# Performance work log

Hardware: AMD Instinct MI355X
Metric: run time of the kernel (lower is better)

The kernel has to match this reference:

```python
import jax, jax.numpy as jnp
import numpy as np

B = 1024      # batch
E = 1024      # encoding_dim
OUT = 34      # 17 joints x 2 coords


def setup_inputs() -> dict:
    key = jax.random.key(0)
    ks = jax.random.split(key, 8)
    s = 0.02  # weight init scale
    return {
        "h": jax.random.normal(ks[0], (B, E), dtype=jnp.float32),
        "c": jax.random.normal(ks[1], (B, E), dtype=jnp.float32),
        "W_ih": jax.random.normal(ks[2], (4 * E, E), dtype=jnp.float32) * s,
        "W_hh": jax.random.normal(ks[3], (4 * E, E), dtype=jnp.float32) * s,
        "b_ih": jax.random.normal(ks[4], (4 * E,), dtype=jnp.float32) * s,
        "b_hh": jax.random.normal(ks[5], (4 * E,), dtype=jnp.float32) * s,
        "W_out": jax.random.normal(ks[6], (OUT, E), dtype=jnp.float32) * s,
        "b_out": jax.random.normal(ks[7], (OUT,), dtype=jnp.float32) * s,
        "future_preds": 10,
    }


def reference(h, c, W_ih, W_hh, b_ih, b_hh, W_out, b_out, future_preds):
    E_ = h.shape[1]
    start = jnp.zeros_like(h)  # zeros=True start token

    def step(carry, _):
        h_t, c_t, x = carry
        # LSTMCell: gates in PyTorch order i, f, g, o
        gates = x @ W_ih.T + b_ih + h_t @ W_hh.T + b_hh  # [B, 4E]
        i = jax.nn.sigmoid(gates[:, 0 * E_:1 * E_])
        f = jax.nn.sigmoid(gates[:, 1 * E_:2 * E_])
        g = jnp.tanh(gates[:, 2 * E_:3 * E_])
        o = jax.nn.sigmoid(gates[:, 3 * E_:4 * E_])
        c_new = f * c_t + i * g
        h_new = o * jnp.tanh(c_new)
        return (h_new, c_new, h_new), h_new

    _, hs = jax.lax.scan(step, (h, c, start), None, length=future_preds)
    # hs: [T, B, E] -> [B, T, E]
    preds = jnp.transpose(hs, (1, 0, 2))
    return preds @ W_out.T + b_out  # [B, T, 34]
```

## Files before the change

### kernel.cpp

```cpp
#include <hip/hip_runtime.h>
#include <cstdint>
#include <cstddef>

#define E_DIM   1024
#define B_DIM   1024
#define T_STEPS 10
#define OUT_DIM 34
#define OUT_PAD 48
#define HSTR    24
#define QK      256
#define WQ_ELEMS (64 * QK)
#define DYN_LDS (2 * WQ_ELEMS * 2 + 128 * HSTR * 2)

typedef __attribute__((ext_vector_type(4))) float  f32x4;
typedef __attribute__((ext_vector_type(8))) __bf16 bf16x8;

__device__ __forceinline__ unsigned short f2bf(float f) {
    unsigned int u = __float_as_uint(f);
    u = (u + 0x7FFFu + ((u >> 16) & 1u)) >> 16;
    return (unsigned short)u;
}
__device__ __forceinline__ float sigmoid_(float x) { return 1.0f / (1.0f + __expf(-x)); }
__device__ __forceinline__ float tanh_(float x)    { return 2.0f / (1.0f + __expf(-2.0f * x)) - 1.0f; }

__global__ void prep_weights_frag(const float* __restrict__ W_ih, const float* __restrict__ W_hh,
                                  unsigned short* __restrict__ WsumF, unsigned short* __restrict__ WhhF) {
    const int bn = blockIdx.x >> 2, qtr = blockIdx.x & 3;
    const int nt = threadIdx.x >> 6, lane = threadIdx.x & 63;
    const int j = lane & 15, q = lane >> 4;
    const int srow = nt * E_DIM + bn * 16 + j;
    const float* wi = W_ih + (size_t)srow * E_DIM;
    const float* wh = W_hh + (size_t)srow * E_DIM;
    const size_t dstb = (size_t)bn * 65536 + (size_t)qtr * 16384 + nt * 512 + lane * 8;
#pragma unroll
    for (int ks8 = 0; ks8 < 8; ++ks8) {
        const int k = qtr * 256 + ks8 * 32 + q * 8;
        float4 i0 = *(const float4*)(wi + k);
        float4 i1 = *(const float4*)(wi + k + 4);
        float4 h0 = *(const float4*)(wh + k);
        float4 h1 = *(const float4*)(wh + k + 4);
        unsigned short* ds = WsumF + dstb + ks8 * 2048;
        unsigned short* dh = WhhF  + dstb + ks8 * 2048;
        ds[0] = f2bf(i0.x + h0.x); ds[1] = f2bf(i0.y + h0.y);
        ds[2] = f2bf(i0.z + h0.z); ds[3] = f2bf(i0.w + h0.w);
        ds[4] = f2bf(i1.x + h1.x); ds[5] = f2bf(i1.y + h1.y);
        ds[6] = f2bf(i1.z + h1.z); ds[7] = f2bf(i1.w + h1.w);
        dh[0] = f2bf(h0.x); dh[1] = f2bf(h0.y); dh[2] = f2bf(h0.z); dh[3] = f2bf(h0.w);
        dh[4] = f2bf(h1.x); dh[5] = f2bf(h1.y); dh[6] = f2bf(h1.z); dh[7] = f2bf(h1.w);
    }
}

__global__ void prep_state(const float* __restrict__ h0, const float* __restrict__ W_out,
                           const float* __restrict__ b_ih, const float* __restrict__ b_hh,
                           unsigned short* __restrict__ hbuf, unsigned short* __restrict__ Woutp,
                           float* __restrict__ bperm) {
    const int b = blockIdx.x;
    const int t = threadIdx.x;
    if (b < 1024) {
        const size_t i = ((size_t)b * 256 + t) * 4;
        float4 hv = *(const float4*)(h0 + i);
        hbuf[i + 0] = f2bf(hv.x);
        hbuf[i + 1] = f2bf(hv.y);
        hbuf[i + 2] = f2bf(hv.z);
        hbuf[i + 3] = f2bf(hv.w);
    } else if (b < 1072) {
        const int o = b - 1024;
        const int k = t * 4;
        float4 w = make_float4(0.f, 0.f, 0.f, 0.f);
        if (o < OUT_DIM) w = *(const float4*)(W_out + (size_t)o * E_DIM + k);
        const size_t dst = (size_t)o * E_DIM + k;
        Woutp[dst + 0] = f2bf(w.x);
        Woutp[dst + 1] = f2bf(w.y);
        Woutp[dst + 2] = f2bf(w.z);
        Woutp[dst + 3] = f2bf(w.w);
    } else {
        const int n = (b - 1072) * 256 + t;
        const int g = (n >> 4) & 3;
        const int e = ((n >> 6) << 4) | (n & 15);
        const int srow = g * E_DIM + e;
        bperm[n] = b_ih[srow] + b_hh[srow];
    }
}

__global__ void prep_c(const float* __restrict__ c0, float* __restrict__ C) {
    const int m = blockIdx.x;
    const int e0 = threadIdx.x * 4;
    float4 v = *(const float4*)(c0 + (size_t)m * E_DIM + e0);
    const int bm = m >> 7, wave = (m >> 5) & 3, mt = (m >> 4) & 1, q = (m >> 2) & 3, r = m & 3;
    const float vv[4] = {v.x, v.y, v.z, v.w};
#pragma unroll
    for (int ii = 0; ii < 4; ++ii) {
        const int e = e0 + ii;
        const int bn = e >> 4, j = e & 15;
        const int lane = q * 16 + j;
        C[(((size_t)(bn * 8 + bm) * 4 + wave) * 64 + lane) * 8 + mt * 4 + r] = vv[ii];
    }
}

__global__ __launch_bounds__(256, 2) void lstm_step(
    const unsigned short* __restrict__ WF,
    const float* __restrict__ bp,
    const unsigned short* __restrict__ Hin,
    float* __restrict__ C,
    unsigned short* __restrict__ Hout)
{
    extern __shared__ __align__(16) unsigned short smem[];
    unsigned short* Wbuf0 = smem;
    unsigned short* Wbuf1 = smem + WQ_ELEMS;
    unsigned short* Ht    = smem + 2 * WQ_ELEMS;

    const int tid  = threadIdx.x;
    const int wave = tid >> 6;
    const int lane = tid & 63;
    const int bn = blockIdx.x;
    const int bm = blockIdx.y;
    const int j  = lane & 15;
    const int q  = lane >> 4;

    f32x4 acc[2][4];
#pragma unroll
    for (int a = 0; a < 2; ++a)
#pragma unroll
        for (int b = 0; b < 4; ++b) acc[a][b] = (f32x4){0.f, 0.f, 0.f, 0.f};

    const int nb = bn * 64 + j;
    const float bi = bp[nb +  0];
    const float bf = bp[nb + 16];
    const float bg = bp[nb + 32];
    const float bo = bp[nb + 48];
    const size_t cbase = (((size_t)(bn * 8 + bm) * 4 + wave) * 64 + lane) * 8;
    float4 cold0 = *(const float4*)(C + cbase);
    float4 cold1 = *(const float4*)(C + cbase + 4);

    const unsigned short* arow0 = Hin + (size_t)(bm * 128 + wave * 32 + j) * E_DIM + q * 8;
    const unsigned short* arow1 = arow0 + (size_t)16 * E_DIM;
    const unsigned short* wsrc  = WF + (size_t)bn * 65536;

    uint4 ra[8][2];
#pragma unroll
    for (int p = 0; p < 8; ++p) {
        ra[p][0] = *(const uint4*)(arow0 + p * 32);
        ra[p][1] = *(const uint4*)(arow1 + p * 32);
    }

    uint4 wreg[8];
#pragma unroll
    for (int i = 0; i < 8; ++i)
        wreg[i] = *(const uint4*)(wsrc + (i * 256 + tid) * 8);
#pragma unroll
    for (int i = 0; i < 8; ++i)
        *(uint4*)(Wbuf0 + (i * 256 + tid) * 8) = wreg[i];
    __syncthreads();

    for (int qtr = 0; qtr < 4; ++qtr) {
        if (qtr < 3) {
#pragma unroll
            for (int i = 0; i < 8; ++i)
                wreg[i] = *(const uint4*)(wsrc + (size_t)(qtr + 1) * WQ_ELEMS + (i * 256 + tid) * 8);
        }
        const unsigned short* wb = ((qtr & 1) ? Wbuf1 : Wbuf0) + lane * 8;
#pragma unroll
        for (int ks8 = 0; ks8 < 8; ++ks8) {
            const int ks = qtr * 8 + ks8;
            bf16x8 av0 = __builtin_bit_cast(bf16x8, ra[ks8][0]);
            bf16x8 av1 = __builtin_bit_cast(bf16x8, ra[ks8][1]);
            bf16x8 bv[4];
#pragma unroll
            for (int nt = 0; nt < 4; ++nt)
                bv[nt] = *(const bf16x8*)(wb + (ks8 * 4 + nt) * 512);
#pragma unroll
            for (int nt = 0; nt < 4; ++nt) {
                acc[0][nt] = __builtin_amdgcn_mfma_f32_16x16x32_bf16(av0, bv[nt], acc[0][nt], 0, 0, 0);
                acc[1][nt] = __builtin_amdgcn_mfma_f32_16x16x32_bf16(av1, bv[nt], acc[1][nt], 0, 0, 0);
            }
            if (ks < 24) {
                ra[ks8][0] = *(const uint4*)(arow0 + (ks + 8) * 32);
                ra[ks8][1] = *(const uint4*)(arow1 + (ks + 8) * 32);
            }
        }
        if (qtr < 3) {
            unsigned short* wn_ = ((qtr + 1) & 1) ? Wbuf1 : Wbuf0;
#pragma unroll
            for (int i = 0; i < 8; ++i)
                *(uint4*)(wn_ + (i * 256 + tid) * 8) = wreg[i];
            __syncthreads();
        }
    }

    float4 cnew[2];
    const float coldv[2][4] = {{cold0.x, cold0.y, cold0.z, cold0.w},
                               {cold1.x, cold1.y, cold1.z, cold1.w}};
#pragma unroll
    for (int mt = 0; mt < 2; ++mt) {
#pragma unroll
        for (int r = 0; r < 4; ++r) {
            const float iv = sigmoid_(acc[mt][0][r] + bi);
            const float fv = sigmoid_(acc[mt][1][r] + bf);
            const float gv = tanh_(acc[mt][2][r] + bg);
            const float ov = sigmoid_(acc[mt][3][r] + bo);
            const float cn = fv * coldv[mt][r] + iv * gv;
            cnew[mt][r] = cn;
            const int rowl = wave * 32 + mt * 16 + q * 4 + r;
            Ht[rowl * HSTR + j] = f2bf(ov * tanh_(cn));
        }
    }
    *(float4*)(C + cbase)     = cnew[0];
    *(float4*)(C + cbase + 4) = cnew[1];
    __syncthreads();

    {
        const int row = tid >> 1, part = tid & 1;
        uint4 v = *(const uint4*)(Ht + row * HSTR + part * 8);
        *(uint4*)(Hout + (size_t)(bm * 128 + row) * E_DIM + bn * 16 + part * 8) = v;
    }
}

__global__ __launch_bounds__(256) void proj_kernel(
    const unsigned short* __restrict__ Hs,
    const unsigned short* __restrict__ Wo,
    const float* __restrict__ b_out,
    float* __restrict__ Out)
{
    __shared__ float red[4][32][OUT_PAD];

    const int tid = threadIdx.x, wave = tid >> 6, lane = tid & 63;
    const int j = lane & 15, q = lane >> 4;
    const int t  = blockIdx.y;
    const int bb = blockIdx.x;
    const unsigned short* Hbase = Hs + ((size_t)t * B_DIM + (size_t)bb * 32) * E_DIM;
    const int k0 = wave * 256;

    f32x4 acc[2][3];
#pragma unroll
    for (int a = 0; a < 2; ++a)
#pragma unroll
        for (int b = 0; b < 3; ++b) acc[a][b] = (f32x4){0.f, 0.f, 0.f, 0.f};

#pragma unroll
    for (int kk = 0; kk < 256; kk += 32) {
        const int kc = k0 + kk + q * 8;
        bf16x8 av[2], bv[3];
#pragma unroll
        for (int mt = 0; mt < 2; ++mt)
            av[mt] = *(const bf16x8*)(Hbase + (size_t)(mt * 16 + j) * E_DIM + kc);
#pragma unroll
        for (int nt = 0; nt < 3; ++nt)
            bv[nt] = *(const bf16x8*)(Wo + (size_t)(nt * 16 + j) * E_DIM + kc);
#pragma unroll
        for (int mt = 0; mt < 2; ++mt)
#pragma unroll
            for (int nt = 0; nt < 3; ++nt)
                acc[mt][nt] = __builtin_amdgcn_mfma_f32_16x16x32_bf16(av[mt], bv[nt], acc[mt][nt], 0, 0, 0);
    }

#pragma unroll
    for (int mt = 0; mt < 2; ++mt)
#pragma unroll
        for (int nt = 0; nt < 3; ++nt)
#pragma unroll
            for (int r = 0; r < 4; ++r)
                red[wave][mt * 16 + q * 4 + r][nt * 16 + j] = acc[mt][nt][r];
    __syncthreads();

#pragma unroll
    for (int ii = 0; ii < 6; ++ii) {
        const int idx = tid * 6 + ii;
        const int row = idx / OUT_PAD, o = idx % OUT_PAD;
        if (o < OUT_DIM) {
            const float s = red[0][row][o] + red[1][row][o] + red[2][row][o] + red[3][row][o];
            Out[((size_t)(bb * 32 + row) * T_STEPS + t) * OUT_DIM + o] = s + b_out[o];
        }
    }
}

extern "C" void kernel_launch(void* const* d_in, const int* in_sizes, int n_in,
                              void* d_out, int out_size, void* d_ws, size_t ws_size,
                              hipStream_t stream) {
    (void)in_sizes; (void)n_in; (void)out_size; (void)ws_size;
    const float* h     = (const float*)d_in[0];
    const float* c     = (const float*)d_in[1];
    const float* W_ih  = (const float*)d_in[2];
    const float* W_hh  = (const float*)d_in[3];
    const float* b_ih  = (const float*)d_in[4];
    const float* b_hh  = (const float*)d_in[5];
    const float* W_out = (const float*)d_in[6];
    const float* b_out = (const float*)d_in[7];
    float* out = (float*)d_out;

    char* ws = (char*)d_ws;
    unsigned short* WsumF = (unsigned short*)(ws + 0);
    unsigned short* WhhF  = (unsigned short*)(ws + 8388608);
    float*          bperm = (float*)(ws + 16777216);
    unsigned short* Woutp = (unsigned short*)(ws + 16842752);
    float*          cbuf  = (float*)(ws + 16941056);
    unsigned short* hs    = (unsigned short*)(ws + 21135360);

    hipFuncSetAttribute((const void*)lstm_step,
                        hipFuncAttributeMaxDynamicSharedMemorySize, DYN_LDS);

    prep_weights_frag<<<256, 256, 0, stream>>>(W_ih, W_hh, WsumF, WhhF);
    prep_state<<<1088, 256, 0, stream>>>(h, W_out, b_ih, b_hh, hs, Woutp, bperm);
    prep_c<<<1024, 256, 0, stream>>>(c, cbuf);

    lstm_step<<<dim3(64, 8), 256, DYN_LDS, stream>>>(WhhF, bperm, hs, cbuf,
                                                     hs + (size_t)B_DIM * E_DIM);
    for (int t = 1; t < T_STEPS; ++t)
        lstm_step<<<dim3(64, 8), 256, DYN_LDS, stream>>>(WsumF, bperm,
                                                         hs + (size_t)t * B_DIM * E_DIM,
                                                         cbuf,
                                                         hs + (size_t)(t + 1) * B_DIM * E_DIM);

    proj_kernel<<<dim3(32, T_STEPS), 256, 0, stream>>>(hs + (size_t)B_DIM * E_DIM,
                                                       Woutp, b_out, out);
}
```

Before: 329.5 us.

## Use eight smaller K-stages with double-buffered A registers and vectorized weight prep

Splits the recurrent GEMM's K loop into eight 128-wide stages instead of four 256-wide ones, halving the LDS weight buffers and the weight registers held per stage. Activation fragments are now double-buffered in registers per stage rather than refilled one slot at a time. The weight prep kernel writes packed 16-byte stores and uses twice as many blocks. The smaller LDS footprint lets the explicit max-dynamic-shared-memory attribute be dropped, though it adds more barriers per kernel.

```diff
diff --git a/kernel.cpp b/kernel.cpp
--- a/kernel.cpp
+++ b/kernel.cpp
@@ -8,9 +8,10 @@
 #define OUT_DIM 34
 #define OUT_PAD 48
 #define HSTR    24
-#define QK      256
-#define WQ_ELEMS (64 * QK)
-#define DYN_LDS (2 * WQ_ELEMS * 2 + 128 * HSTR * 2)
+#define EK      128
+#define WE_ELEMS (64 * EK)
+#define DYN_LDS (2 * WE_ELEMS * 2 + 128 * HSTR * 2)
+#define LDP     40
 
 typedef __attribute__((ext_vector_type(4))) float  f32x4;
 typedef __attribute__((ext_vector_type(8))) __bf16 bf16x8;
@@ -25,28 +26,29 @@
 
 __global__ void prep_weights_frag(const float* __restrict__ W_ih, const float* __restrict__ W_hh,
                                   unsigned short* __restrict__ WsumF, unsigned short* __restrict__ WhhF) {
-    const int bn = blockIdx.x >> 2, qtr = blockIdx.x & 3;
+    const int bn = blockIdx.x >> 3, E = blockIdx.x & 7;
     const int nt = threadIdx.x >> 6, lane = threadIdx.x & 63;
     const int j = lane & 15, q = lane >> 4;
     const int srow = nt * E_DIM + bn * 16 + j;
     const float* wi = W_ih + (size_t)srow * E_DIM;
     const float* wh = W_hh + (size_t)srow * E_DIM;
-    const size_t dstb = (size_t)bn * 65536 + (size_t)qtr * 16384 + nt * 512 + lane * 8;
-#pragma unroll
-    for (int ks8 = 0; ks8 < 8; ++ks8) {
-        const int k = qtr * 256 + ks8 * 32 + q * 8;
+    const size_t dstb = (size_t)bn * 65536 + (size_t)E * 8192 + nt * 512 + lane * 8;
+#pragma unroll
+    for (int ks8 = 0; ks8 < 4; ++ks8) {
+        const int k = E * 128 + ks8 * 32 + q * 8;
         float4 i0 = *(const float4*)(wi + k);
         float4 i1 = *(const float4*)(wi + k + 4);
         float4 h0 = *(const float4*)(wh + k);
         float4 h1 = *(const float4*)(wh + k + 4);
-        unsigned short* ds = WsumF + dstb + ks8 * 2048;
-        unsigned short* dh = WhhF  + dstb + ks8 * 2048;
-        ds[0] = f2bf(i0.x + h0.x); ds[1] = f2bf(i0.y + h0.y);
-        ds[2] = f2bf(i0.z + h0.z); ds[3] = f2bf(i0.w + h0.w);
-        ds[4] = f2bf(i1.x + h1.x); ds[5] = f2bf(i1.y + h1.y);
-        ds[6] = f2bf(i1.z + h1.z); ds[7] = f2bf(i1.w + h1.w);
-        dh[0] = f2bf(h0.x); dh[1] = f2bf(h0.y); dh[2] = f2bf(h0.z); dh[3] = f2bf(h0.w);
-        dh[4] = f2bf(h1.x); dh[5] = f2bf(h1.y); dh[6] = f2bf(h1.z); dh[7] = f2bf(h1.w);
+        unsigned short s[8], hh[8];
+        s[0] = f2bf(i0.x + h0.x); s[1] = f2bf(i0.y + h0.y);
+        s[2] = f2bf(i0.z + h0.z); s[3] = f2bf(i0.w + h0.w);
+        s[4] = f2bf(i1.x + h1.x); s[5] = f2bf(i1.y + h1.y);
+        s[6] = f2bf(i1.z + h1.z); s[7] = f2bf(i1.w + h1.w);
+        hh[0] = f2bf(h0.x); hh[1] = f2bf(h0.y); hh[2] = f2bf(h0.z); hh[3] = f2bf(h0.w);
+        hh[4] = f2bf(h1.x); hh[5] = f2bf(h1.y); hh[6] = f2bf(h1.z); hh[7] = f2bf(h1.w);
+        *(uint4*)(WsumF + dstb + ks8 * 2048) = *(const uint4*)s;
+        *(uint4*)(WhhF  + dstb + ks8 * 2048) = *(const uint4*)hh;
     }
 }
 
@@ -105,9 +107,8 @@
     unsigned short* __restrict__ Hout)
 {
     extern __shared__ __align__(16) unsigned short smem[];
-    unsigned short* Wbuf0 = smem;
-    unsigned short* Wbuf1 = smem + WQ_ELEMS;
-    unsigned short* Ht    = smem + 2 * WQ_ELEMS;
+    unsigned short* Wb[2] = { smem, smem + WE_ELEMS };
+    unsigned short* Ht    = smem + 2 * WE_ELEMS;
 
     const int tid  = threadIdx.x;
     const int wave = tid >> 6;
@@ -136,34 +137,40 @@
     const unsigned short* arow1 = arow0 + (size_t)16 * E_DIM;
     const unsigned short* wsrc  = WF + (size_t)bn * 65536;
 
-    uint4 ra[8][2];
-#pragma unroll
-    for (int p = 0; p < 8; ++p) {
-        ra[p][0] = *(const uint4*)(arow0 + p * 32);
-        ra[p][1] = *(const uint4*)(arow1 + p * 32);
-    }
-
-    uint4 wreg[8];
-#pragma unroll
-    for (int i = 0; i < 8; ++i)
+    uint4 ra[2][4][2];
+    uint4 wreg[4];
+
+#pragma unroll
+    for (int s = 0; s < 4; ++s) {
+        ra[0][s][0] = *(const uint4*)(arow0 + s * 32);
+        ra[0][s][1] = *(const uint4*)(arow1 + s * 32);
+    }
+#pragma unroll
+    for (int i = 0; i < 4; ++i)
         wreg[i] = *(const uint4*)(wsrc + (i * 256 + tid) * 8);
 #pragma unroll
-    for (int i = 0; i < 8; ++i)
-        *(uint4*)(Wbuf0 + (i * 256 + tid) * 8) = wreg[i];
+    for (int i = 0; i < 4; ++i)
+        *(uint4*)(Wb[0] + (i * 256 + tid) * 8) = wreg[i];
     __syncthreads();
 
-    for (int qtr = 0; qtr < 4; ++qtr) {
-        if (qtr < 3) {
-#pragma unroll
-            for (int i = 0; i < 8; ++i)
-                wreg[i] = *(const uint4*)(wsrc + (size_t)(qtr + 1) * WQ_ELEMS + (i * 256 + tid) * 8);
-        }
-        const unsigned short* wb = ((qtr & 1) ? Wbuf1 : Wbuf0) + lane * 8;
-#pragma unroll
-        for (int ks8 = 0; ks8 < 8; ++ks8) {
-            const int ks = qtr * 8 + ks8;
-            bf16x8 av0 = __builtin_bit_cast(bf16x8, ra[ks8][0]);
-            bf16x8 av1 = __builtin_bit_cast(bf16x8, ra[ks8][1]);
+#pragma unroll
+    for (int E = 0; E < 8; ++E) {
+        const int cur = E & 1;
+        if (E < 7) {
+#pragma unroll
+            for (int s = 0; s < 4; ++s) {
+                ra[1 - cur][s][0] = *(const uint4*)(arow0 + (E + 1) * EK + s * 32);
+                ra[1 - cur][s][1] = *(const uint4*)(arow1 + (E + 1) * EK + s * 32);
+            }
+#pragma unroll
+            for (int i = 0; i < 4; ++i)
+                wreg[i] = *(const uint4*)(wsrc + (size_t)(E + 1) * WE_ELEMS + (i * 256 + tid) * 8);
+        }
+        const unsigned short* wb = Wb[cur] + lane * 8;
+#pragma unroll
+        for (int ks8 = 0; ks8 < 4; ++ks8) {
+            bf16x8 av0 = __builtin_bit_cast(bf16x8, ra[cur][ks8][0]);
+            bf16x8 av1 = __builtin_bit_cast(bf16x8, ra[cur][ks8][1]);
             bf16x8 bv[4];
 #pragma unroll
             for (int nt = 0; nt < 4; ++nt)
@@ -173,15 +180,11 @@
                 acc[0][nt] = __builtin_amdgcn_mfma_f32_16x16x32_bf16(av0, bv[nt], acc[0][nt], 0, 0, 0);
                 acc[1][nt] = __builtin_amdgcn_mfma_f32_16x16x32_bf16(av1, bv[nt], acc[1][nt], 0, 0, 0);
             }
-            if (ks < 24) {
-                ra[ks8][0] = *(const uint4*)(arow0 + (ks + 8) * 32);
-                ra[ks8][1] = *(const uint4*)(arow1 + (ks + 8) * 32);
-            }
-        }
-        if (qtr < 3) {
-            unsigned short* wn_ = ((qtr + 1) & 1) ? Wbuf1 : Wbuf0;
-#pragma unroll
-            for (int i = 0; i < 8; ++i)
+        }
+        if (E < 7) {
+            unsigned short* wn_ = Wb[1 - cur];
+#pragma unroll
+            for (int i = 0; i < 4; ++i)
                 *(uint4*)(wn_ + (i * 256 + tid) * 8) = wreg[i];
             __syncthreads();
         }
@@ -295,10 +298,7 @@
     float*          cbuf  = (float*)(ws + 16941056);
     unsigned short* hs    = (unsigned short*)(ws + 21135360);
 
-    hipFuncSetAttribute((const void*)lstm_step,
-                        hipFuncAttributeMaxDynamicSharedMemorySize, DYN_LDS);
-
-    prep_weights_frag<<<256, 256, 0, stream>>>(W_ih, W_hh, WsumF, WhhF);
+    prep_weights_frag<<<512, 256, 0, stream>>>(W_ih, W_hh, WsumF, WhhF);
     prep_state<<<1088, 256, 0, stream>>>(h, W_out, b_ih, b_hh, hs, Woutp, bperm);
     prep_c<<<1024, 256, 0, stream>>>(c, cbuf);
 
```

Result: no change. 330.8 us (+0.4%).
